# Optimization experiments

Measured on AMD Instinct MI355X. Metric: run time of the kernel, lower is better.

## Reference

```python
import jax, jax.numpy as jnp
import numpy as np

B, DIM, HEADS, H, W = 4, 192, 6, 256, 256
C = DIM // HEADS  # channels per head
DN = ('NCHW', 'OIHW', 'NCHW')


def conv2d(x, w, b, padding='VALID', groups=1):
    y = jax.lax.conv_general_dilated(x, w, (1, 1), padding,
                                     dimension_numbers=DN,
                                     feature_group_count=groups)
    return y + b[None, :, None, None]


def setup_inputs() -> dict:
    key = jax.random.key(0)
    ks = jax.random.split(key, 8)
    s = 0.02
    return {
        'x': jax.random.normal(ks[0], (B, DIM, H, W), jnp.float32),
        'qkv_w': jax.random.normal(ks[1], (3 * DIM, DIM, 1, 1), jnp.float32) * s,
        'qkv_b': jnp.zeros((3 * DIM,), jnp.float32),
        'dw_w': jax.random.normal(ks[2], (3 * DIM, 1, 3, 3), jnp.float32) * s,
        'dw_b': jnp.zeros((3 * DIM,), jnp.float32),
        'proj_w': jax.random.normal(ks[3], (DIM, DIM, 1, 1), jnp.float32) * s,
        'proj_b': jnp.zeros((DIM,), jnp.float32),
        'temperature': jnp.ones((HEADS, 1, 1, 1), jnp.float32),
    }


def reference(x, qkv_w, qkv_b, dw_w, dw_b, proj_w, proj_b, temperature):
    # qkv projection: 1x1 conv then 3x3 depthwise conv
    qkv = conv2d(x, qkv_w, qkv_b)
    qkv = conv2d(qkv, dw_w, dw_b, padding='SAME', groups=3 * DIM)
    q, k, v = jnp.split(qkv, 3, axis=1)  # each (B, DIM, H, W)

    def heads(t):
        return t.reshape(B, HEADS, C, H, W)
    q, k, v = heads(q), heads(k), heads(v)

    # L2-normalize along W (matches F.normalize eps=1e-12)
    eps = 1e-12
    q = q / jnp.maximum(jnp.linalg.norm(q, axis=-1, keepdims=True), eps)
    k = k / jnp.maximum(jnp.linalg.norm(k, axis=-1, keepdims=True), eps)

    # per-channel HxH attention, contraction over W; temperature broadcasts over head
    attn = jnp.einsum('bncxw,bncyw->bncxy', q, k) * temperature  # (B,HEADS,C,H,H)
    attn = jax.nn.softmax(attn, axis=-1)
    out = jnp.einsum('bncxy,bncyw->bncxw', attn, v)  # (B,HEADS,C,H,W)

    out = out.reshape(B, DIM, H, W)
    return conv2d(out, proj_w, proj_b)
```

## Files before the change

kernel.cpp:

```cpp
#include <hip/hip_runtime.h>
#include <hip/hip_bf16.h>
#include <math.h>


#define HW 65536
#define IMW 256

typedef short bf16x8 __attribute__((ext_vector_type(8)));
typedef float f32x4  __attribute__((ext_vector_type(4)));

__device__ __forceinline__ float bf2f(ushort u) {
    return __uint_as_float((uint)u << 16);
}
__device__ __forceinline__ ushort f2bf(float f) {
    uint i = __float_as_uint(f);
    return (ushort)((i + 0x7FFFu + ((i >> 16) & 1u)) >> 16);
}

__device__ __forceinline__ void gload16(const ushort* g, ushort* l) {
    __builtin_amdgcn_global_load_lds(
        (const __attribute__((address_space(1))) void*)g,
        (__attribute__((address_space(3))) void*)l,
        16, 0, 0);
}

__global__ __launch_bounds__(256) void cvt_f32_bf16(const float* __restrict__ s,
                                                    ushort* __restrict__ d, int n)
{
    int i = blockIdx.x * 256 + threadIdx.x;
    if (i < n) d[i] = f2bf(s[i]);
}

__global__ __launch_bounds__(256) void cvt_transpose_f32(const float* __restrict__ src,
                                                         ushort* __restrict__ dst,
                                                         int R, int C,
                                                         long ssS, long ssD)
{
    __shared__ ushort Ls[64][72];
    int t = threadIdx.x;
    long z = blockIdx.z;
    src += z * ssS; dst += z * ssD;
    int c0 = blockIdx.x * 64, r0 = blockIdx.y * 64;
    {
        int r = t >> 2, cs = t & 3;
        const float* gp = src + (size_t)(r0 + r) * C + c0 + cs * 16;
        ushort tmp[16];
        #pragma unroll
        for (int q = 0; q < 4; ++q) {
            float4 v = *(const float4*)(gp + q * 4);
            tmp[q*4+0] = f2bf(v.x); tmp[q*4+1] = f2bf(v.y);
            tmp[q*4+2] = f2bf(v.z); tmp[q*4+3] = f2bf(v.w);
        }
        *(uint4*)&Ls[r][cs * 16]     = *(uint4*)&tmp[0];
        *(uint4*)&Ls[r][cs * 16 + 8] = *(uint4*)&tmp[8];
    }
    __syncthreads();
    {
        int cc = t & 63, seg = t >> 6;
        ushort tmp[16];
        #pragma unroll
        for (int j = 0; j < 16; ++j) tmp[j] = Ls[seg * 16 + j][cc];
        ushort* op = dst + (size_t)(c0 + cc) * R + r0 + seg * 16;
        *(uint4*)(op)     = *(uint4*)&tmp[0];
        *(uint4*)(op + 8) = *(uint4*)&tmp[8];
    }
}

__global__ __launch_bounds__(256) void transpose_bf16(const ushort* __restrict__ src,
                                                      ushort* __restrict__ dst,
                                                      int R, int C,
                                                      long ssS, long ssD)
{
    __shared__ ushort Ls[64][72];
    int t = threadIdx.x;
    long z = blockIdx.z;
    src += z * ssS; dst += z * ssD;
    int c0 = blockIdx.x * 64, r0 = blockIdx.y * 64;
    {
        int r = t >> 2, cs = t & 3;
        const ushort* gp = src + (size_t)(r0 + r) * C + c0 + cs * 16;
        *(uint4*)&Ls[r][cs * 16]     = *(const uint4*)(gp);
        *(uint4*)&Ls[r][cs * 16 + 8] = *(const uint4*)(gp + 8);
    }
    __syncthreads();
    {
        int cc = t & 63, seg = t >> 6;
        ushort tmp[16];
        #pragma unroll
        for (int j = 0; j < 16; ++j) tmp[j] = Ls[seg * 16 + j][cc];
        ushort* op = dst + (size_t)(c0 + cc) * R + r0 + seg * 16;
        *(uint4*)(op)     = *(uint4*)&tmp[0];
        *(uint4*)(op + 8) = *(uint4*)&tmp[8];
    }
}

__global__ __launch_bounds__(256) void transpose_v(const ushort* __restrict__ post,
                                                   ushort* __restrict__ vt)
{
    __shared__ ushort Ls[64][72];
    int t = threadIdx.x;
    int s = blockIdx.z;
    int b = s / 192, r = s - b * 192;
    const ushort* src = post + ((size_t)b * 576 + 384 + r) * HW;
    ushort*       dst = vt + (size_t)s * HW;
    int c0 = blockIdx.x * 64, r0 = blockIdx.y * 64;
    {
        int rr = t >> 2, cs = t & 3;
        const ushort* gp = src + (size_t)(r0 + rr) * IMW + c0 + cs * 16;
        *(uint4*)&Ls[rr][cs * 16]     = *(const uint4*)(gp);
        *(uint4*)&Ls[rr][cs * 16 + 8] = *(const uint4*)(gp + 8);
    }
    __syncthreads();
    {
        int cc = t & 63, seg = t >> 6;
        ushort tmp[16];
        #pragma unroll
        for (int j = 0; j < 16; ++j) tmp[j] = Ls[seg * 16 + j][cc];
        ushort* op = dst + (size_t)(c0 + cc) * IMW + r0 + seg * 16;
        *(uint4*)(op)     = *(uint4*)&tmp[0];
        *(uint4*)(op + 8) = *(uint4*)&tmp[8];
    }
}

__global__ __launch_bounds__(256) void gemm_mfma(const ushort* __restrict__ A, int lda, long sliceA,
                                                 const ushort* __restrict__ B, int ldb, long sliceB,
                                                 void* __restrict__ Dp, int ldd, long sliceD,
                                                 const float* __restrict__ bias,
                                                 int K, int outF32, int NM, int NN)
{
    int lin = blockIdx.x;
    int r8 = lin & 7, kk_ = lin >> 3;
    int m = kk_ % NM, fg = kk_ / NM;
    int g = fg * 8 + r8;
    int nt_ = g % NN;
    long z = g / NN;
    int m0 = m * 64;
    int n0 = nt_ * 256;

    __shared__ ushort Ws[64][32];
    __shared__ ushort Xs[256][32];
    int t = threadIdx.x, wv = t >> 6, lane = t & 63;
    int fr = lane & 15, sg = lane >> 4;
    A += z * sliceA; B += z * sliceB;

    int rl   = wv * 16 + (lane >> 2);
    int chnk = (lane & 3) ^ ((lane >> 3) & 3);
    const ushort* srcA = A + (size_t)(m0 + rl) * lda + chnk * 8;
    const ushort* srcB0 = B + (size_t)(n0 +       rl) * ldb + chnk * 8;
    const ushort* srcB1 = B + (size_t)(n0 +  64 + rl) * ldb + chnk * 8;
    const ushort* srcB2 = B + (size_t)(n0 + 128 + rl) * ldb + chnk * 8;
    const ushort* srcB3 = B + (size_t)(n0 + 192 + rl) * ldb + chnk * 8;

    int sp = sg ^ ((fr >> 1) & 3);

    f32x4 acc[4][4];
    #pragma unroll
    for (int i = 0; i < 4; ++i)
        #pragma unroll
        for (int j = 0; j < 4; ++j) acc[i][j] = (f32x4){0.f, 0.f, 0.f, 0.f};

    for (int k0 = 0; k0 < K; k0 += 32) {
        gload16(srcA  + k0, &Ws[wv * 16][0]);
        gload16(srcB0 + k0, &Xs[      wv * 16][0]);
        gload16(srcB1 + k0, &Xs[ 64 + wv * 16][0]);
        gload16(srcB2 + k0, &Xs[128 + wv * 16][0]);
        gload16(srcB3 + k0, &Xs[192 + wv * 16][0]);
        __syncthreads();
        bf16x8 a[4];
        #pragma unroll
        for (int i = 0; i < 4; ++i)
            a[i] = *(const bf16x8*)&Ws[i * 16 + fr][sp * 8];
        #pragma unroll
        for (int j = 0; j < 4; ++j) {
            bf16x8 b = *(const bf16x8*)&Xs[wv * 64 + j * 16 + fr][sp * 8];
            #pragma unroll
            for (int i = 0; i < 4; ++i)
                acc[i][j] = __builtin_amdgcn_mfma_f32_16x16x32_bf16(a[i], b, acc[i][j], 0, 0, 0);
        }
        __syncthreads();
    }

    int nw0 = n0 + wv * 64;
    int rbase = sg * 4;
    if (outF32) {
        float* D = (float*)Dp + z * sliceD;
        #pragma unroll
        for (int i = 0; i < 4; ++i) {
            #pragma unroll
            for (int r_ = 0; r_ < 4; ++r_) {
                int mrow = m0 + i * 16 + rbase + r_;
                float bv = bias ? bias[mrow] : 0.f;
                #pragma unroll
                for (int j = 0; j < 4; ++j)
                    D[(size_t)mrow * ldd + nw0 + j * 16 + fr] = acc[i][j][r_] + bv;
            }
        }
    } else {
        ushort* D = (ushort*)Dp + z * sliceD;
        #pragma unroll
        for (int i = 0; i < 4; ++i) {
            #pragma unroll
            for (int r_ = 0; r_ < 4; ++r_) {
                int mrow = m0 + i * 16 + rbase + r_;
                float bv = bias ? bias[mrow] : 0.f;
                #pragma unroll
                for (int j = 0; j < 4; ++j)
                    D[(size_t)mrow * ldd + nw0 + j * 16 + fr] = f2bf(acc[i][j][r_] + bv);
            }
        }
    }
}

__global__ __launch_bounds__(256) void attn_fused(const ushort* __restrict__ post,
                                                  const ushort* __restrict__ vt,
                                                  const float* __restrict__ temp,
                                                  ushort* __restrict__ O)
{
    __shared__ ushort Ws[64][32];
    __shared__ ushort Xs[256][32];
    __shared__ ushort Ps[64][264];
    int t = threadIdx.x, wv = t >> 6, lane = t & 63;
    int fr = lane & 15, sg = lane >> 4;
    int lin = blockIdx.x;
    int r8 = lin & 7, k_ = lin >> 3;
    int mtile = k_ & 3, fg = k_ >> 2;
    int s = fg * 8 + r8;
    int b = s / 192, ch = s - b * 192;
    const ushort* Aq = post + ((size_t)b * 576 + ch) * HW;
    const ushort* Bk = Aq + (size_t)192 * HW;
    const ushort* Vt = vt + (size_t)s * HW;
    int m0 = mtile * 64;

    int rl   = wv * 16 + (lane >> 2);
    int chnk = (lane & 3) ^ ((lane >> 3) & 3);
    int sp   = sg ^ ((fr >> 1) & 3);
    const ushort* srcQ  = Aq + (size_t)(m0 + rl) * IMW + chnk * 8;
    const ushort* srcK0 = Bk + (size_t)(      rl) * IMW + chnk * 8;
    const ushort* srcK1 = Bk + (size_t)( 64 + rl) * IMW + chnk * 8;
    const ushort* srcK2 = Bk + (size_t)(128 + rl) * IMW + chnk * 8;
    const ushort* srcK3 = Bk + (size_t)(192 + rl) * IMW + chnk * 8;
    const ushort* srcV0 = Vt + (size_t)(      rl) * IMW + chnk * 8;
    const ushort* srcV1 = Vt + (size_t)( 64 + rl) * IMW + chnk * 8;
    const ushort* srcV2 = Vt + (size_t)(128 + rl) * IMW + chnk * 8;
    const ushort* srcV3 = Vt + (size_t)(192 + rl) * IMW + chnk * 8;

    f32x4 acc[16];
    #pragma unroll
    for (int i = 0; i < 16; ++i) acc[i] = (f32x4){0.f, 0.f, 0.f, 0.f};

    for (int k0 = 0; k0 < 256; k0 += 32) {
        gload16(srcQ  + k0, &Ws[wv * 16][0]);
        gload16(srcK0 + k0, &Xs[      wv * 16][0]);
        gload16(srcK1 + k0, &Xs[ 64 + wv * 16][0]);
        gload16(srcK2 + k0, &Xs[128 + wv * 16][0]);
        gload16(srcK3 + k0, &Xs[192 + wv * 16][0]);
        __syncthreads();
        bf16x8 a = *(const bf16x8*)&Ws[wv * 16 + fr][sp * 8];
        #pragma unroll
        for (int nt = 0; nt < 16; ++nt) {
            bf16x8 bfrag = *(const bf16x8*)&Xs[nt * 16 + fr][sp * 8];
            acc[nt] = __builtin_amdgcn_mfma_f32_16x16x32_bf16(a, bfrag, acc[nt], 0, 0, 0);
        }
        __syncthreads();
    }

    float tv = temp[ch >> 5];
    #pragma unroll
    for (int r_ = 0; r_ < 4; ++r_) {
        float v[16];
        float mx = -3.4e38f;
        #pragma unroll
        for (int nt = 0; nt < 16; ++nt) { v[nt] = acc[nt][r_] * tv; mx = fmaxf(mx, v[nt]); }
        #pragma unroll
        for (int sh = 1; sh < 16; sh <<= 1) mx = fmaxf(mx, __shfl_xor(mx, sh, 64));
        float sum = 0.f;
        #pragma unroll
        for (int nt = 0; nt < 16; ++nt) { v[nt] = __expf(v[nt] - mx); sum += v[nt]; }
        #pragma unroll
        for (int sh = 1; sh < 16; sh <<= 1) sum += __shfl_xor(sum, sh, 64);
        float inv = 1.f / sum;
        int ml = wv * 16 + sg * 4 + r_;
        #pragma unroll
        for (int nt = 0; nt < 16; ++nt)
            Ps[ml][fr + nt * 16] = f2bf(v[nt] * inv);
    }

    f32x4 acc2[16];
    #pragma unroll
    for (int i = 0; i < 16; ++i) acc2[i] = (f32x4){0.f, 0.f, 0.f, 0.f};

    for (int y0 = 0; y0 < 256; y0 += 32) {
        gload16(srcV0 + y0, &Xs[      wv * 16][0]);
        gload16(srcV1 + y0, &Xs[ 64 + wv * 16][0]);
        gload16(srcV2 + y0, &Xs[128 + wv * 16][0]);
        gload16(srcV3 + y0, &Xs[192 + wv * 16][0]);
        __syncthreads();
        bf16x8 a = *(const bf16x8*)&Ps[wv * 16 + fr][y0 + sg * 8];
        #pragma unroll
        for (int nt = 0; nt < 16; ++nt) {
            bf16x8 bfrag = *(const bf16x8*)&Xs[nt * 16 + fr][sp * 8];
            acc2[nt] = __builtin_amdgcn_mfma_f32_16x16x32_bf16(a, bfrag, acc2[nt], 0, 0, 0);
        }
        __syncthreads();
    }

    ushort* Op = O + (size_t)s * HW;
    int mrow = m0 + wv * 16 + sg * 4;
    #pragma unroll
    for (int r_ = 0; r_ < 4; ++r_) {
        #pragma unroll
        for (int nt = 0; nt < 16; ++nt)
            Op[(size_t)(mrow + r_) * IMW + fr + nt * 16] = f2bf(acc2[nt][r_]);
    }
}

__global__ __launch_bounds__(256) void dw3x3_l2norm(const ushort* __restrict__ in,
                                                    const float* __restrict__ w,
                                                    const float* __restrict__ bias,
                                                    ushort* __restrict__ out)
{
    int t = threadIdx.x;
    int lane = t & 63, wv = t >> 6;
    int ch = blockIdx.y;
    int r0 = blockIdx.x * 16 + wv * 4;
    const ushort* img  = in  + ((size_t)blockIdx.z * 576 + ch) * HW;
    ushort*       outp = out + ((size_t)blockIdx.z * 576 + ch) * HW;
    int px = lane * 4;

    float rv[6][4], lv[6], rx[6];
    #pragma unroll
    for (int i = 0; i < 6; ++i) {
        int rr = r0 - 1 + i;
        if ((unsigned)rr <= 255u) {
            ushort4 cv = *(const ushort4*)&img[(size_t)rr * IMW + px];
            rv[i][0] = bf2f(cv.x); rv[i][1] = bf2f(cv.y);
            rv[i][2] = bf2f(cv.z); rv[i][3] = bf2f(cv.w);
        } else {
            rv[i][0] = rv[i][1] = rv[i][2] = rv[i][3] = 0.f;
        }
        float l = __shfl_up(rv[i][3], 1, 64);
        lv[i] = (lane == 0) ? 0.f : l;
        float r = __shfl_down(rv[i][0], 1, 64);
        rx[i] = (lane == 63) ? 0.f : r;
    }

    const float* wch = w + ch * 9;
    float bv = bias[ch];
    bool do_norm = (ch < 384);

    #pragma unroll
    for (int j = 0; j < 4; ++j) {
        float a0 = bv, a1 = bv, a2 = bv, a3 = bv;
        #pragma unroll
        for (int dy = 0; dy < 3; ++dy) {
            int i = j + dy;
            float w0 = wch[dy * 3], w1 = wch[dy * 3 + 1], w2 = wch[dy * 3 + 2];
            a0 += lv[i]    * w0 + rv[i][0] * w1 + rv[i][1] * w2;
            a1 += rv[i][0] * w0 + rv[i][1] * w1 + rv[i][2] * w2;
            a2 += rv[i][1] * w0 + rv[i][2] * w1 + rv[i][3] * w2;
            a3 += rv[i][2] * w0 + rv[i][3] * w1 + rx[i]    * w2;
        }
        if (do_norm) {
            float ss = a0 * a0 + a1 * a1 + a2 * a2 + a3 * a3;
            #pragma unroll
            for (int m = 1; m < 64; m <<= 1) ss += __shfl_xor(ss, m, 64);
            float inv = 1.0f / fmaxf(sqrtf(ss), 1e-12f);
            a0 *= inv; a1 *= inv; a2 *= inv; a3 *= inv;
        }
        ushort4 o;
        o.x = f2bf(a0); o.y = f2bf(a1); o.z = f2bf(a2); o.w = f2bf(a3);
        *(ushort4*)&outp[(size_t)(r0 + j) * IMW + px] = o;
    }
}

extern "C" void kernel_launch(void* const* d_in, const int* in_sizes, int n_in,
                              void* d_out, int out_size, void* d_ws, size_t ws_size,
                              hipStream_t stream)
{
    const float* x      = (const float*)d_in[0];
    const float* qkv_w  = (const float*)d_in[1];
    const float* qkv_b  = (const float*)d_in[2];
    const float* dw_w   = (const float*)d_in[3];
    const float* dw_b   = (const float*)d_in[4];
    const float* proj_w = (const float*)d_in[5];
    const float* proj_b = (const float*)d_in[6];
    const float* temp   = (const float*)d_in[7];
    float* out = (float*)d_out;

    const size_t off_wq   = 0;
    const size_t off_wp   = 110592;
    const size_t off_pre  = 262144;
    const size_t off_post = off_pre + (size_t)4 * 576 * HW;
    const size_t off_xt   = off_post + (size_t)4 * 576 * HW;
    const size_t total_us = off_xt + (size_t)4 * 192 * HW;
    if (ws_size < total_us * sizeof(ushort)) return;

    ushort* wsb  = (ushort*)d_ws;
    ushort* wq   = wsb + off_wq;
    ushort* wp   = wsb + off_wp;
    ushort* pre  = wsb + off_pre;
    ushort* post = wsb + off_post;
    ushort* xt   = wsb + off_xt;
    ushort* Obuf = pre;
    ushort* Otb  = pre + (size_t)4 * 192 * HW;

    const long SL = (long)192 * HW;

    cvt_f32_bf16<<<dim3(432), 256, 0, stream>>>(qkv_w, wq, 110592);
    cvt_f32_bf16<<<dim3(144), 256, 0, stream>>>(proj_w, wp, 36864);

    cvt_transpose_f32<<<dim3(1024, 3, 4), 256, 0, stream>>>(x, xt, 192, HW, SL, SL);
    gemm_mfma<<<dim3(9 * 256 * 4), 256, 0, stream>>>(wq, 192, 0, xt, 192, SL,
                                                     pre, HW, (long)576 * HW,
                                                     qkv_b, 192, 0, 9, 256);
    dw3x3_l2norm<<<dim3(16, 576, 4), 256, 0, stream>>>(pre, dw_w, dw_b, post);
    transpose_v<<<dim3(4, 4, 768), 256, 0, stream>>>(post, xt);
    attn_fused<<<dim3(4 * 768), 256, 0, stream>>>(post, xt, temp, Obuf);
    transpose_bf16<<<dim3(1024, 3, 4), 256, 0, stream>>>(Obuf, Otb, 192, HW, SL, SL);
    gemm_mfma<<<dim3(3 * 256 * 4), 256, 0, stream>>>(wp, 192, 0, Otb, 192, SL,
                                                     out, HW, SL,
                                                     proj_b, 192, 1, 3, 256);
}
```

Baseline: 700.9 us.

## Make 1x1-conv GEMM persistent over four N tiles with double-buffered B loads

Each GEMM block now keeps its full 64x192 weight tile resident in LDS and walks four consecutive 256-column N tiles. B tiles are double-buffered, so the next K slice's global-to-LDS load is issued before computing on the current one, replacing the load-sync-compute pattern. This cuts redundant weight loads and block count by four and aims to overlap memory with MFMA work. In exchange it uses more LDS per block, launches fewer blocks (possibly lower occupancy or tail imbalance), hardcodes K=192, and writes the epilogue inside the loop.

```diff
diff --git a/kernel.cpp b/kernel.cpp
--- a/kernel.cpp
+++ b/kernel.cpp
@@ -126,19 +126,19 @@
                                                  const ushort* __restrict__ B, int ldb, long sliceB,
                                                  void* __restrict__ Dp, int ldd, long sliceD,
                                                  const float* __restrict__ bias,
-                                                 int K, int outF32, int NM, int NN)
+                                                 int outF32, int NM, int NGRP)
 {
     int lin = blockIdx.x;
-    int r8 = lin & 7, kk_ = lin >> 3;
-    int m = kk_ % NM, fg = kk_ / NM;
+    int r8 = lin & 7, k_ = lin >> 3;
+    int m = k_ % NM, fg = k_ / NM;
     int g = fg * 8 + r8;
-    int nt_ = g % NN;
-    long z = g / NN;
+    int ngrp = g % NGRP;
+    long z = g / NGRP;
     int m0 = m * 64;
-    int n0 = nt_ * 256;
-
-    __shared__ ushort Ws[64][32];
-    __shared__ ushort Xs[256][32];
+    int nbase = ngrp * 1024;
+
+    __shared__ ushort As[6][64][32];
+    __shared__ ushort Bs[2][256][32];
     int t = threadIdx.x, wv = t >> 6, lane = t & 63;
     int fr = lane & 15, sg = lane >> 4;
     A += z * sliceA; B += z * sliceB;
@@ -146,10 +146,7 @@
     int rl   = wv * 16 + (lane >> 2);
     int chnk = (lane & 3) ^ ((lane >> 3) & 3);
     const ushort* srcA = A + (size_t)(m0 + rl) * lda + chnk * 8;
-    const ushort* srcB0 = B + (size_t)(n0 +       rl) * ldb + chnk * 8;
-    const ushort* srcB1 = B + (size_t)(n0 +  64 + rl) * ldb + chnk * 8;
-    const ushort* srcB2 = B + (size_t)(n0 + 128 + rl) * ldb + chnk * 8;
-    const ushort* srcB3 = B + (size_t)(n0 + 192 + rl) * ldb + chnk * 8;
+    const ushort* srcB = B + (size_t)(nbase + rl) * ldb + chnk * 8;
 
     int sp = sg ^ ((fr >> 1) & 3);
 
@@ -159,54 +156,72 @@
         #pragma unroll
         for (int j = 0; j < 4; ++j) acc[i][j] = (f32x4){0.f, 0.f, 0.f, 0.f};
 
-    for (int k0 = 0; k0 < K; k0 += 32) {
-        gload16(srcA  + k0, &Ws[wv * 16][0]);
-        gload16(srcB0 + k0, &Xs[      wv * 16][0]);
-        gload16(srcB1 + k0, &Xs[ 64 + wv * 16][0]);
-        gload16(srcB2 + k0, &Xs[128 + wv * 16][0]);
-        gload16(srcB3 + k0, &Xs[192 + wv * 16][0]);
-        __syncthreads();
+    #pragma unroll
+    for (int p = 0; p < 6; ++p)
+        gload16(srcA + p * 32, &As[p][wv * 16][0]);
+    #pragma unroll
+    for (int q = 0; q < 4; ++q)
+        gload16(srcB + (size_t)(q * 64) * ldb, &Bs[0][q * 64 + wv * 16][0]);
+    __syncthreads();
+
+    for (int it = 0; it < 24; ++it) {
+        int kit = it % 6;
+        int cur = it & 1;
+        if (it + 1 < 24) {
+            int ng1 = (it + 1) / 6;
+            int kc1 = ((it + 1) % 6) * 32;
+            #pragma unroll
+            for (int q = 0; q < 4; ++q)
+                gload16(srcB + (size_t)(ng1 * 256 + q * 64) * ldb + kc1,
+                        &Bs[cur ^ 1][q * 64 + wv * 16][0]);
+        }
         bf16x8 a[4];
         #pragma unroll
         for (int i = 0; i < 4; ++i)
-            a[i] = *(const bf16x8*)&Ws[i * 16 + fr][sp * 8];
+            a[i] = *(const bf16x8*)&As[kit][i * 16 + fr][sp * 8];
         #pragma unroll
         for (int j = 0; j < 4; ++j) {
-            bf16x8 b = *(const bf16x8*)&Xs[wv * 64 + j * 16 + fr][sp * 8];
+            bf16x8 b = *(const bf16x8*)&Bs[cur][wv * 64 + j * 16 + fr][sp * 8];
             #pragma unroll
             for (int i = 0; i < 4; ++i)
                 acc[i][j] = __builtin_amdgcn_mfma_f32_16x16x32_bf16(a[i], b, acc[i][j], 0, 0, 0);
         }
         __syncthreads();
-    }
-
-    int nw0 = n0 + wv * 64;
-    int rbase = sg * 4;
-    if (outF32) {
-        float* D = (float*)Dp + z * sliceD;
-        #pragma unroll
-        for (int i = 0; i < 4; ++i) {
+
+        if (kit == 5) {
+            int nw0 = nbase + (it / 6) * 256 + wv * 64;
+            int rbase = sg * 4;
+            if (outF32) {
+                float* D = (float*)Dp + z * sliceD;
+                #pragma unroll
+                for (int i = 0; i < 4; ++i) {
+                    #pragma unroll
+                    for (int r_ = 0; r_ < 4; ++r_) {
+                        int mrow = m0 + i * 16 + rbase + r_;
+                        float bv = bias ? bias[mrow] : 0.f;
+                        #pragma unroll
+                        for (int j = 0; j < 4; ++j)
+                            D[(size_t)mrow * ldd + nw0 + j * 16 + fr] = acc[i][j][r_] + bv;
+                    }
+                }
+            } else {
+                ushort* D = (ushort*)Dp + z * sliceD;
+                #pragma unroll
+                for (int i = 0; i < 4; ++i) {
+                    #pragma unroll
+                    for (int r_ = 0; r_ < 4; ++r_) {
+                        int mrow = m0 + i * 16 + rbase + r_;
+                        float bv = bias ? bias[mrow] : 0.f;
+                        #pragma unroll
+                        for (int j = 0; j < 4; ++j)
+                            D[(size_t)mrow * ldd + nw0 + j * 16 + fr] = f2bf(acc[i][j][r_] + bv);
+                    }
+                }
+            }
             #pragma unroll
-            for (int r_ = 0; r_ < 4; ++r_) {
-                int mrow = m0 + i * 16 + rbase + r_;
-                float bv = bias ? bias[mrow] : 0.f;
+            for (int i = 0; i < 4; ++i)
                 #pragma unroll
-                for (int j = 0; j < 4; ++j)
-                    D[(size_t)mrow * ldd + nw0 + j * 16 + fr] = acc[i][j][r_] + bv;
-            }
-        }
-    } else {
-        ushort* D = (ushort*)Dp + z * sliceD;
-        #pragma unroll
-        for (int i = 0; i < 4; ++i) {
-            #pragma unroll
-            for (int r_ = 0; r_ < 4; ++r_) {
-                int mrow = m0 + i * 16 + rbase + r_;
-                float bv = bias ? bias[mrow] : 0.f;
-                #pragma unroll
-                for (int j = 0; j < 4; ++j)
-                    D[(size_t)mrow * ldd + nw0 + j * 16 + fr] = f2bf(acc[i][j][r_] + bv);
-            }
+                for (int j = 0; j < 4; ++j) acc[i][j] = (f32x4){0.f, 0.f, 0.f, 0.f};
         }
     }
 }
@@ -410,14 +425,14 @@
     cvt_f32_bf16<<<dim3(144), 256, 0, stream>>>(proj_w, wp, 36864);
 
     cvt_transpose_f32<<<dim3(1024, 3, 4), 256, 0, stream>>>(x, xt, 192, HW, SL, SL);
-    gemm_mfma<<<dim3(9 * 256 * 4), 256, 0, stream>>>(wq, 192, 0, xt, 192, SL,
-                                                     pre, HW, (long)576 * HW,
-                                                     qkv_b, 192, 0, 9, 256);
+    gemm_mfma<<<dim3(9 * 64 * 4), 256, 0, stream>>>(wq, 192, 0, xt, 192, SL,
+                                                    pre, HW, (long)576 * HW,
+                                                    qkv_b, 0, 9, 64);
     dw3x3_l2norm<<<dim3(16, 576, 4), 256, 0, stream>>>(pre, dw_w, dw_b, post);
     transpose_v<<<dim3(4, 4, 768), 256, 0, stream>>>(post, xt);
     attn_fused<<<dim3(4 * 768), 256, 0, stream>>>(post, xt, temp, Obuf);
     transpose_bf16<<<dim3(1024, 3, 4), 256, 0, stream>>>(Obuf, Otb, 192, HW, SL, SL);
-    gemm_mfma<<<dim3(3 * 256 * 4), 256, 0, stream>>>(wp, 192, 0, Otb, 192, SL,
-                                                     out, HW, SL,
-                                                     proj_b, 192, 1, 3, 256);
-}
+    gemm_mfma<<<dim3(3 * 64 * 4), 256, 0, stream>>>(wp, 192, 0, Otb, 192, SL,
+                                                    out, HW, SL,
+                                                    proj_b, 1, 3, 64);
+}
```

Result: slower. 765.9 us (+9.3%).
